# Kernel optimization log

Hardware: AMD Instinct MI355X
Metric: run time of the kernel (lower is better)

Reference implementation:

```python
import jax, jax.numpy as jnp
import numpy as np

DROPOUT_RATE = 0.5
CONF_THRESH = 0.85
IGNORE_VALUE = 2
EPS = 1e-07


def setup_inputs() -> dict:
    key = jax.random.key(0)
    k1, k2 = jax.random.split(key)
    B, H, W = 16, 1024, 1024
    pred = jax.random.uniform(k1, (B, H, W), dtype=jnp.float32)
    mask = jax.random.randint(k2, (B, H, W), 0, 3, dtype=jnp.int32)
    return {"pred": pred, "mask": mask}


def _training_need_score(pred, gt, confidence):
    # Higher = needs more training: CW=4, UW=3, UC=2, CC=1 (+/- confidence bonus)
    is_correct = (pred > 0.5) == (gt == 1.0)
    is_conf = confidence > CONF_THRESH
    score = jnp.where(is_conf & is_correct, 1.0,
            jnp.where(~is_conf & is_correct, 2.0,
            jnp.where(~is_conf & ~is_correct, 3.0, 4.0))).astype(pred.dtype)
    bonus = (confidence - 0.5) * 0.5
    return jnp.where(is_correct, score - bonus, score + bonus)


def _dynamic_masks(pred, mask):
    # Vectorized equivalent of the per-batch nonzero/argsort/scatter loop:
    # rank annotated pixels per batch by descending need-score; top n_train -> train.
    B, H, W = mask.shape
    annotated = (mask != IGNORE_VALUE).reshape(B, H * W)
    gt = mask.astype(pred.dtype)
    confidence = jnp.maximum(pred, 1.0 - pred)
    scores = _training_need_score(pred, gt, confidence).reshape(B, H * W)
    neg_inf = jnp.asarray(-jnp.inf, scores.dtype)
    masked_scores = jnp.where(annotated, scores, neg_inf)
    order = jnp.argsort(-masked_scores, axis=1)          # descending score order
    rank = jnp.argsort(order, axis=1)                    # rank of each pixel in that order
    n_points = annotated.sum(axis=1)
    n_train = (n_points.astype(jnp.float32) * (1.0 - DROPOUT_RATE)).astype(jnp.int32)
    train = annotated & (rank < n_train[:, None])
    holdout = annotated & ~train
    return train.reshape(B, H, W), holdout.reshape(B, H, W)


def reference(pred, mask):
    if pred.ndim == 4 and pred.shape[1] == 1:
        pred = pred[:, 0]
    train_mask, holdout_mask = _dynamic_masks(pred, mask)
    gt = mask.astype(pred.dtype)
    p = jnp.clip(pred, EPS, 1.0 - EPS)
    bce = -(gt * jnp.log(p) + (1.0 - gt) * jnp.log(1.0 - p))
    tm = train_mask.astype(pred.dtype)
    loss = (bce * tm).sum() / (tm.sum() + EPS)
    return loss, train_mask, holdout_mask
```

## Files before the change

kernel.cpp:

```cpp
#include <hip/hip_runtime.h>
#include <stdint.h>

#define NBATCH 16
#define HW_ (1 << 20)
#define TPB 256

#define NBPB_H 32
#define TPB_H 512
#define EPB_H (HW_ / NBPB_H)
#define ITER_H (EPB_H / (TPB_H * 4))

#define NBINS 8192
#define FBASE 0x3F400

#define NBPB_F 256
#define FCHUNK (HW_ / NBPB_F)

#define CAND_CAP 32768
#define LCAP 512
#define TIE_CAP 4096
#define CNT_STRIDE 64

typedef float f4v __attribute__((ext_vector_type(4)));

struct BParams {
    unsigned int k;
    unsigned int bin1f;
    unsigned int r;
    unsigned int mode;
};

__device__ __forceinline__ unsigned int score_bits(float p, int m) {
    bool correct = (p > 0.5f) == (m == 1);
    float conf = fmaxf(p, 1.0f - p);
    float base = correct ? ((conf > 0.85f) ? 1.0f : 2.0f)
                         : ((conf > 0.85f) ? 4.0f : 3.0f);
    float bonus = (conf - 0.5f) * 0.5f;
    float s = correct ? (base - bonus) : (base + bonus);
    return __float_as_uint(s);
}

__global__ void k_hist1(const float4* __restrict__ pred4, const int4* __restrict__ mask4,
                        unsigned int* __restrict__ hist1) {
    __shared__ unsigned int lh[NBINS];
    int b = blockIdx.x / NBPB_H;
    int blk = blockIdx.x % NBPB_H;
    for (int i = threadIdx.x; i < NBINS; i += TPB_H) lh[i] = 0;
    __syncthreads();
    int l4base = blk * (EPB_H / 4);
    for (int j = 0; j < ITER_H; j++) {
        int i4l = l4base + j * TPB_H + threadIdx.x;
        size_t g4 = (size_t)b * (HW_ / 4) + i4l;
        float4 p = pred4[g4];
        int4 m = mask4[g4];
        float pa[4] = {p.x, p.y, p.z, p.w};
        int ma[4] = {m.x, m.y, m.z, m.w};
#pragma unroll
        for (int l = 0; l < 4; l++) {
            if (ma[l] != 2) {
                unsigned int sb = score_bits(pa[l], ma[l]);
                int fb = (int)(sb >> 12) - FBASE;
                fb = min(max(fb, 0), NBINS - 1);
                atomicAdd(&lh[fb], 1u);
            }
        }
    }
    __syncthreads();
    for (int i = threadIdx.x; i < NBINS; i += TPB_H)
        if (lh[i]) atomicAdd(&hist1[b * NBINS + i], lh[i]);
}

__global__ void k_find1(const unsigned int* __restrict__ hist1, BParams* prm) {
    int b = blockIdx.x;
    int t = threadIdx.x;
    __shared__ unsigned int cs_[257];
    const unsigned int* h = hist1 + (size_t)b * NBINS;
    {
        const uint4* h4 = (const uint4*)(h + t * 32);
        unsigned int s = 0;
#pragma unroll
        for (int j = 0; j < 8; j++) { uint4 v = h4[j]; s += v.x + v.y + v.z + v.w; }
        cs_[t] = s;
        if (t == 0) cs_[256] = 0;
    }
    __syncthreads();
    for (int off = 1; off < 256; off <<= 1) {
        unsigned int a = (t + off < 256) ? cs_[t + off] : 0u;
        __syncthreads();
        cs_[t] += a;
        __syncthreads();
    }
    unsigned int n = cs_[0];
    unsigned int k = (unsigned int)(int)((float)n * 0.5f);
    if (k == 0) {
        if (t == 0) {
            BParams P;
            P.k = 0; P.bin1f = 0xFFFFFFFFu; P.r = 0; P.mode = 0;
            prm[b] = P;
        }
        return;
    }
    if (cs_[t] >= k && cs_[t + 1] < k) {
        unsigned int cum = cs_[t + 1];
        for (int j = 31; j >= 0; j--) {
            unsigned int hb = h[t * 32 + j];
            if (cum + hb >= k) {
                BParams P;
                P.k = k;
                P.bin1f = (unsigned int)(FBASE + t * 32 + j);
                P.r = k - cum;
                P.mode = 1;
                prm[b] = P;
                break;
            }
            cum += hb;
        }
    }
}

__global__ void k_main(const float4* __restrict__ pred4, const int4* __restrict__ mask4,
                       const BParams* __restrict__ prm, float* __restrict__ out,
                       float* __restrict__ partials, unsigned int* __restrict__ cand_cnt,
                       unsigned int* __restrict__ cand_idx, unsigned int* __restrict__ cand_sb,
                       float* __restrict__ cand_bce) {
    int b = blockIdx.x / NBPB_F;
    int blk = blockIdx.x % NBPB_F;
    BParams P = prm[b];
    unsigned int target = P.bin1f;
    __shared__ unsigned int lcode[FCHUNK / 4];
    __shared__ float red[TPB];
    __shared__ unsigned int l_idx[LCAP];
    __shared__ unsigned int l_sb[LCAP];
    __shared__ float l_bce[LCAP];
    __shared__ unsigned int lcnt;
    __shared__ unsigned int gbase;
    if (threadIdx.x == 0) lcnt = 0;
    __syncthreads();
    float acc = 0.0f;
    int ibase = blk * FCHUNK;
    for (int j = 0; j < FCHUNK / (TPB * 4); j++) {
        int v = j * TPB + threadIdx.x;
        size_t g4 = (size_t)b * (HW_ / 4) + (ibase / 4) + v;
        float4 p = pred4[g4];
        int4 m = mask4[g4];
        float pa[4] = {p.x, p.y, p.z, p.w};
        int ma[4] = {m.x, m.y, m.z, m.w};
        unsigned int cw = 0;
#pragma unroll
        for (int l = 0; l < 4; l++) {
            bool ann = (ma[l] != 2);
            unsigned int sb = score_bits(pa[l], ma[l]);
            unsigned int fine = sb >> 12;
            bool tr = ann && (fine > target);
            bool amb = ann && (fine == target);
            unsigned int code = (tr ? 1u : 0u) | ((ann && !tr) ? 2u : 0u);
            cw |= code << (8 * l);
            float bce = 0.0f;
            if (tr || amb) {
                float pc = fminf(fmaxf(pa[l], 1e-7f), 1.0f - 1e-7f);
                bce = (ma[l] == 1) ? -__logf(pc) : -__logf(1.0f - pc);
            }
            if (tr) acc += bce;
            if (amb) {
                unsigned int p0 = atomicAdd(&lcnt, 1u);
                if (p0 < LCAP) {
                    l_idx[p0] = (unsigned int)(ibase + v * 4 + l);
                    l_sb[p0] = sb;
                    l_bce[p0] = bce;
                } else {
                    unsigned int gp = atomicAdd(&cand_cnt[b * CNT_STRIDE], 1u);
                    if (gp < CAND_CAP) {
                        size_t o = (size_t)b * CAND_CAP + gp;
                        cand_idx[o] = (unsigned int)(ibase + v * 4 + l);
                        cand_sb[o] = sb;
                        cand_bce[o] = bce;
                    }
                }
            }
        }
        lcode[v] = cw;
    }
    __syncthreads();
    unsigned int n = min(lcnt, (unsigned int)LCAP);
    if (threadIdx.x == 0 && n > 0)
        gbase = atomicAdd(&cand_cnt[b * CNT_STRIDE], n);
    __syncthreads();
    for (unsigned int i = threadIdx.x; i < n; i += TPB) {
        unsigned int pos = gbase + i;
        if (pos < CAND_CAP) {
            size_t o = (size_t)b * CAND_CAP + pos;
            cand_idx[o] = l_idx[i];
            cand_sb[o] = l_sb[i];
            cand_bce[o] = l_bce[i];
        }
    }
    float* trout = out + 1;
    float* hoout = out + 1 + (size_t)NBATCH * HW_;
    size_t Gbase = (size_t)b * HW_ + (size_t)ibase;
    for (int v = threadIdx.x; v < FCHUNK / 4 - 1; v += TPB) {
        unsigned int w0 = lcode[v];
        unsigned int w1 = lcode[v + 1];
        unsigned int c0 = (w0 >> 24) & 0xFFu;
        unsigned int c1 = w1 & 0xFFu;
        unsigned int c2 = (w1 >> 8) & 0xFFu;
        unsigned int c3 = (w1 >> 16) & 0xFFu;
        int e = 3 + 4 * v;
        f4v tv = { (float)(c0 & 1u), (float)(c1 & 1u), (float)(c2 & 1u), (float)(c3 & 1u) };
        f4v hv = { (float)((c0 >> 1) & 1u), (float)((c1 >> 1) & 1u),
                   (float)((c2 >> 1) & 1u), (float)((c3 >> 1) & 1u) };
        __builtin_nontemporal_store(tv, (f4v*)(trout + Gbase + e));
        __builtin_nontemporal_store(hv, (f4v*)(hoout + Gbase + e));
    }
    if (threadIdx.x < 3) {
        unsigned int c = (lcode[0] >> (8 * threadIdx.x)) & 0xFFu;
        trout[Gbase + threadIdx.x] = (float)(c & 1u);
        hoout[Gbase + threadIdx.x] = (float)((c >> 1) & 1u);
    }
    if (threadIdx.x == 3) {
        unsigned int c = (lcode[FCHUNK / 4 - 1] >> 24) & 0xFFu;
        trout[Gbase + FCHUNK - 1] = (float)(c & 1u);
        hoout[Gbase + FCHUNK - 1] = (float)((c >> 1) & 1u);
    }
    red[threadIdx.x] = acc;
    __syncthreads();
    for (int off = TPB / 2; off > 0; off >>= 1) {
        if (threadIdx.x < off) red[threadIdx.x] += red[threadIdx.x + off];
        __syncthreads();
    }
    if (threadIdx.x == 0) partials[blockIdx.x] = red[0];
}

__global__ void k_fixup(const unsigned int* __restrict__ cand_cnt,
                        const unsigned int* __restrict__ cand_idx,
                        const unsigned int* __restrict__ cand_sb,
                        const float* __restrict__ cand_bce,
                        const BParams* __restrict__ prm, float* __restrict__ out,
                        float* __restrict__ tie_partials) {
    int b = blockIdx.x;
    int t = threadIdx.x;
    __shared__ unsigned int h[4096];
    __shared__ unsigned int cs_[257];
    __shared__ unsigned int tie_idx[TIE_CAP];
    __shared__ unsigned int misc[8];
    __shared__ float red[TPB];
    BParams P = prm[b];
    if (P.mode == 0) {
        if (t == 0) tie_partials[b] = 0.0f;
        return;
    }
    unsigned int C = cand_cnt[b * CNT_STRIDE];
    if (C > CAND_CAP) C = CAND_CAP;
    const unsigned int* ci = cand_idx + (size_t)b * CAND_CAP;
    const unsigned int* cs = cand_sb + (size_t)b * CAND_CAP;
    const float* cb = cand_bce + (size_t)b * CAND_CAP;
    for (int i = t; i < 4096; i += TPB) h[i] = 0;
    if (t < 8) misc[t] = (t == 4) ? 0xFFFFFFFFu : 0u;
    __syncthreads();
    for (unsigned int i = t; i < C; i += TPB)
        atomicAdd(&h[cs[i] & 0xFFFu], 1u);
    __syncthreads();
    {
        unsigned int gs = 0;
#pragma unroll
        for (int j = 0; j < 16; j++) gs += h[t * 16 + j];
        cs_[t] = gs;
        if (t == 0) cs_[256] = 0;
    }
    __syncthreads();
    for (int off = 1; off < 256; off <<= 1) {
        unsigned int a = (t + off < 256) ? cs_[t + off] : 0u;
        __syncthreads();
        cs_[t] += a;
        __syncthreads();
    }
    if (cs_[t] >= P.r && cs_[t + 1] < P.r) {
        unsigned int cum = cs_[t + 1];
        for (int j = 15; j >= 0; j--) {
            unsigned int hb = h[t * 16 + j];
            if (cum + hb >= P.r) {
                unsigned int T = P.r - cum;
                misc[0] = (unsigned int)(t * 16 + j);
                misc[1] = T;
                misc[2] = (T == hb) ? 1u : 0u;
                break;
            }
            cum += hb;
        }
    }
    __syncthreads();
    unsigned int vstar = misc[0], T = misc[1];
    bool allTies = (misc[2] != 0);
    unsigned int idxcut;
    if (allTies) {
        idxcut = 0xFFFFFFFFu;
    } else {
        for (unsigned int i = t; i < C; i += TPB) {
            if ((cs[i] & 0xFFFu) == vstar) {
                unsigned int p = atomicAdd(&misc[3], 1u);
                if (p < TIE_CAP) tie_idx[p] = ci[i];
            }
        }
        __syncthreads();
        unsigned int E2 = misc[3];
        if (E2 > TIE_CAP) E2 = TIE_CAP;
        for (unsigned int i = t; i < E2; i += TPB) {
            unsigned int vi = tie_idx[i];
            unsigned int cnt = 0;
            for (unsigned int j = 0; j < E2; j++) cnt += (tie_idx[j] < vi) ? 1u : 0u;
            if (cnt == T - 1) misc[4] = vi;
        }
        __syncthreads();
        idxcut = misc[4];
    }
    float acc = 0.0f;
    float* trout = out + 1;
    float* hoout = out + 1 + (size_t)NBATCH * HW_;
    size_t base = (size_t)b * HW_;
    for (unsigned int i = t; i < C; i += TPB) {
        unsigned int low = cs[i] & 0xFFFu;
        bool tr = (low > vstar) || (low == vstar && ci[i] <= idxcut);
        if (tr) {
            trout[base + ci[i]] = 1.0f;
            hoout[base + ci[i]] = 0.0f;
            acc += cb[i];
        }
    }
    red[t] = acc;
    __syncthreads();
    for (int off = TPB / 2; off > 0; off >>= 1) {
        if (t < off) red[t] += red[t + off];
        __syncthreads();
    }
    if (t == 0) tie_partials[b] = red[0];
}

__global__ void k_loss(const float* __restrict__ partials, const float* __restrict__ tie_partials,
                       const BParams* __restrict__ prm, float* __restrict__ out) {
    __shared__ double red[TPB];
    double s = 0.0;
    for (int i = threadIdx.x; i < NBATCH * NBPB_F; i += TPB) s += (double)partials[i];
    if (threadIdx.x < NBATCH) s += (double)tie_partials[threadIdx.x];
    red[threadIdx.x] = s;
    __syncthreads();
    for (int off = TPB / 2; off > 0; off >>= 1) {
        if (threadIdx.x < off) red[threadIdx.x] += red[threadIdx.x + off];
        __syncthreads();
    }
    if (threadIdx.x == 0) {
        unsigned long long den = 0;
        for (int b = 0; b < NBATCH; b++) den += prm[b].k;
        float denf = (float)den + 1e-7f;
        out[0] = (float)red[0] / denf;
    }
}

extern "C" void kernel_launch(void* const* d_in, const int* in_sizes, int n_in,
                              void* d_out, int out_size, void* d_ws, size_t ws_size,
                              hipStream_t stream) {
    const float4* pred4 = (const float4*)d_in[0];
    const int4* mask4 = (const int4*)d_in[1];
    float* out = (float*)d_out;

    unsigned int* hist1 = (unsigned int*)d_ws;
    unsigned int* cand_cnt = hist1 + NBATCH * NBINS;
    BParams* prm = (BParams*)(cand_cnt + NBATCH * CNT_STRIDE);
    float* partials = (float*)(prm + NBATCH);
    float* tie_partials = partials + NBATCH * NBPB_F;
    unsigned int* cand_idx = (unsigned int*)(tie_partials + NBATCH);
    unsigned int* cand_sb = cand_idx + NBATCH * CAND_CAP;
    float* cand_bce = (float*)(cand_sb + NBATCH * CAND_CAP);

    size_t zero_bytes = (size_t)(NBATCH * NBINS + NBATCH * CNT_STRIDE) * 4;
    hipMemsetAsync(d_ws, 0, zero_bytes, stream);

    k_hist1<<<dim3(NBATCH * NBPB_H), dim3(TPB_H), 0, stream>>>(pred4, mask4, hist1);
    k_find1<<<dim3(NBATCH), dim3(TPB), 0, stream>>>(hist1, prm);
    k_main<<<dim3(NBATCH * NBPB_F), dim3(TPB), 0, stream>>>(pred4, mask4, prm, out, partials,
                                                            cand_cnt, cand_idx, cand_sb, cand_bce);
    k_fixup<<<dim3(NBATCH), dim3(TPB), 0, stream>>>(cand_cnt, cand_idx, cand_sb, cand_bce,
                                                    prm, out, tie_partials);
    k_loss<<<dim3(1), dim3(TPB), 0, stream>>>(partials, tie_partials, prm, out);
}
```

Measured before the change: 286.0 us.

## Fuse find and loss kernels into predecessors via last-block atomic counters

Replaces the separate k_find1 and k_loss launches with last-block-done patterns. The final histogram block of each batch does the threshold search, and the final fixup block does the global loss reduction, using atomic counters and agent-scope loads. It also doubles the histogram blocks per batch to give the pass more parallelism. This removes two kernel launches and their gaps, at the cost of fences, counter atomics and more global histogram atomics.

New measurement: 427.1 us. 49.3% more time.

```diff
diff --git a/kernel.cpp b/kernel.cpp
--- a/kernel.cpp
+++ b/kernel.cpp
@@ -5,7 +5,7 @@
 #define HW_ (1 << 20)
 #define TPB 256
 
-#define NBPB_H 32
+#define NBPB_H 64
 #define TPB_H 512
 #define EPB_H (HW_ / NBPB_H)
 #define ITER_H (EPB_H / (TPB_H * 4))
@@ -40,16 +40,27 @@
     return __float_as_uint(s);
 }
 
+__device__ __forceinline__ unsigned int agent_load_u32(const unsigned int* p) {
+    return __hip_atomic_load(p, __ATOMIC_RELAXED, __HIP_MEMORY_SCOPE_AGENT);
+}
+__device__ __forceinline__ float agent_load_f32(const float* p) {
+    return __hip_atomic_load(p, __ATOMIC_RELAXED, __HIP_MEMORY_SCOPE_AGENT);
+}
+
 __global__ void k_hist1(const float4* __restrict__ pred4, const int4* __restrict__ mask4,
-                        unsigned int* __restrict__ hist1) {
+                        unsigned int* __restrict__ hist1, unsigned int* __restrict__ done_h,
+                        BParams* __restrict__ prm) {
     __shared__ unsigned int lh[NBINS];
+    __shared__ unsigned int cs_[TPB_H + 1];
+    __shared__ unsigned int lasth;
     int b = blockIdx.x / NBPB_H;
     int blk = blockIdx.x % NBPB_H;
-    for (int i = threadIdx.x; i < NBINS; i += TPB_H) lh[i] = 0;
+    int t = threadIdx.x;
+    for (int i = t; i < NBINS; i += TPB_H) lh[i] = 0;
     __syncthreads();
     int l4base = blk * (EPB_H / 4);
     for (int j = 0; j < ITER_H; j++) {
-        int i4l = l4base + j * TPB_H + threadIdx.x;
+        int i4l = l4base + j * TPB_H + t;
         size_t g4 = (size_t)b * (HW_ / 4) + i4l;
         float4 p = pred4[g4];
         int4 m = mask4[g4];
@@ -66,26 +77,25 @@
         }
     }
     __syncthreads();
-    for (int i = threadIdx.x; i < NBINS; i += TPB_H)
+    for (int i = t; i < NBINS; i += TPB_H)
         if (lh[i]) atomicAdd(&hist1[b * NBINS + i], lh[i]);
-}
-
-__global__ void k_find1(const unsigned int* __restrict__ hist1, BParams* prm) {
-    int b = blockIdx.x;
-    int t = threadIdx.x;
-    __shared__ unsigned int cs_[257];
+    __threadfence();
+    __syncthreads();
+    if (t == 0) lasth = (atomicAdd(&done_h[b], 1u) == NBPB_H - 1) ? 1u : 0u;
+    __syncthreads();
+    if (!lasth) return;
+    __threadfence();
     const unsigned int* h = hist1 + (size_t)b * NBINS;
     {
-        const uint4* h4 = (const uint4*)(h + t * 32);
         unsigned int s = 0;
 #pragma unroll
-        for (int j = 0; j < 8; j++) { uint4 v = h4[j]; s += v.x + v.y + v.z + v.w; }
+        for (int j = 0; j < 16; j++) s += agent_load_u32(&h[t * 16 + j]);
         cs_[t] = s;
-        if (t == 0) cs_[256] = 0;
-    }
-    __syncthreads();
-    for (int off = 1; off < 256; off <<= 1) {
-        unsigned int a = (t + off < 256) ? cs_[t + off] : 0u;
+        if (t == 0) cs_[TPB_H] = 0;
+    }
+    __syncthreads();
+    for (int off = 1; off < TPB_H; off <<= 1) {
+        unsigned int a = (t + off < TPB_H) ? cs_[t + off] : 0u;
         __syncthreads();
         cs_[t] += a;
         __syncthreads();
@@ -102,12 +112,12 @@
     }
     if (cs_[t] >= k && cs_[t + 1] < k) {
         unsigned int cum = cs_[t + 1];
-        for (int j = 31; j >= 0; j--) {
-            unsigned int hb = h[t * 32 + j];
+        for (int j = 15; j >= 0; j--) {
+            unsigned int hb = agent_load_u32(&h[t * 16 + j]);
             if (cum + hb >= k) {
                 BParams P;
                 P.k = k;
-                P.bin1f = (unsigned int)(FBASE + t * 32 + j);
+                P.bin1f = (unsigned int)(FBASE + t * 16 + j);
                 P.r = k - cum;
                 P.mode = 1;
                 prm[b] = P;
@@ -235,7 +245,9 @@
                         const unsigned int* __restrict__ cand_sb,
                         const float* __restrict__ cand_bce,
                         const BParams* __restrict__ prm, float* __restrict__ out,
-                        float* __restrict__ tie_partials) {
+                        float* __restrict__ tie_partials,
+                        const float* __restrict__ partials,
+                        unsigned int* __restrict__ done_f) {
     int b = blockIdx.x;
     int t = threadIdx.x;
     __shared__ unsigned int h[4096];
@@ -243,114 +255,118 @@
     __shared__ unsigned int tie_idx[TIE_CAP];
     __shared__ unsigned int misc[8];
     __shared__ float red[TPB];
+    __shared__ double redd[TPB];
+    __shared__ unsigned int lastf;
     BParams P = prm[b];
-    if (P.mode == 0) {
-        if (t == 0) tie_partials[b] = 0.0f;
-        return;
-    }
-    unsigned int C = cand_cnt[b * CNT_STRIDE];
-    if (C > CAND_CAP) C = CAND_CAP;
-    const unsigned int* ci = cand_idx + (size_t)b * CAND_CAP;
-    const unsigned int* cs = cand_sb + (size_t)b * CAND_CAP;
-    const float* cb = cand_bce + (size_t)b * CAND_CAP;
-    for (int i = t; i < 4096; i += TPB) h[i] = 0;
-    if (t < 8) misc[t] = (t == 4) ? 0xFFFFFFFFu : 0u;
-    __syncthreads();
-    for (unsigned int i = t; i < C; i += TPB)
-        atomicAdd(&h[cs[i] & 0xFFFu], 1u);
-    __syncthreads();
-    {
-        unsigned int gs = 0;
+    float tieval = 0.0f;
+    if (P.mode != 0) {
+        unsigned int C = cand_cnt[b * CNT_STRIDE];
+        if (C > CAND_CAP) C = CAND_CAP;
+        const unsigned int* ci = cand_idx + (size_t)b * CAND_CAP;
+        const unsigned int* cs = cand_sb + (size_t)b * CAND_CAP;
+        const float* cb = cand_bce + (size_t)b * CAND_CAP;
+        for (int i = t; i < 4096; i += TPB) h[i] = 0;
+        if (t < 8) misc[t] = (t == 4) ? 0xFFFFFFFFu : 0u;
+        __syncthreads();
+        for (unsigned int i = t; i < C; i += TPB)
+            atomicAdd(&h[cs[i] & 0xFFFu], 1u);
+        __syncthreads();
+        {
+            unsigned int gs = 0;
 #pragma unroll
-        for (int j = 0; j < 16; j++) gs += h[t * 16 + j];
-        cs_[t] = gs;
-        if (t == 0) cs_[256] = 0;
-    }
-    __syncthreads();
-    for (int off = 1; off < 256; off <<= 1) {
-        unsigned int a = (t + off < 256) ? cs_[t + off] : 0u;
-        __syncthreads();
-        cs_[t] += a;
-        __syncthreads();
-    }
-    if (cs_[t] >= P.r && cs_[t + 1] < P.r) {
-        unsigned int cum = cs_[t + 1];
-        for (int j = 15; j >= 0; j--) {
-            unsigned int hb = h[t * 16 + j];
-            if (cum + hb >= P.r) {
-                unsigned int T = P.r - cum;
-                misc[0] = (unsigned int)(t * 16 + j);
-                misc[1] = T;
-                misc[2] = (T == hb) ? 1u : 0u;
-                break;
-            }
-            cum += hb;
-        }
-    }
-    __syncthreads();
-    unsigned int vstar = misc[0], T = misc[1];
-    bool allTies = (misc[2] != 0);
-    unsigned int idxcut;
-    if (allTies) {
-        idxcut = 0xFFFFFFFFu;
-    } else {
+            for (int j = 0; j < 16; j++) gs += h[t * 16 + j];
+            cs_[t] = gs;
+            if (t == 0) cs_[256] = 0;
+        }
+        __syncthreads();
+        for (int off = 1; off < 256; off <<= 1) {
+            unsigned int a = (t + off < 256) ? cs_[t + off] : 0u;
+            __syncthreads();
+            cs_[t] += a;
+            __syncthreads();
+        }
+        if (cs_[t] >= P.r && cs_[t + 1] < P.r) {
+            unsigned int cum = cs_[t + 1];
+            for (int j = 15; j >= 0; j--) {
+                unsigned int hb = h[t * 16 + j];
+                if (cum + hb >= P.r) {
+                    unsigned int T = P.r - cum;
+                    misc[0] = (unsigned int)(t * 16 + j);
+                    misc[1] = T;
+                    misc[2] = (T == hb) ? 1u : 0u;
+                    break;
+                }
+                cum += hb;
+            }
+        }
+        __syncthreads();
+        unsigned int vstar = misc[0], T = misc[1];
+        bool allTies = (misc[2] != 0);
+        unsigned int idxcut;
+        if (allTies) {
+            idxcut = 0xFFFFFFFFu;
+        } else {
+            for (unsigned int i = t; i < C; i += TPB) {
+                if ((cs[i] & 0xFFFu) == vstar) {
+                    unsigned int p = atomicAdd(&misc[3], 1u);
+                    if (p < TIE_CAP) tie_idx[p] = ci[i];
+                }
+            }
+            __syncthreads();
+            unsigned int E2 = misc[3];
+            if (E2 > TIE_CAP) E2 = TIE_CAP;
+            for (unsigned int i = t; i < E2; i += TPB) {
+                unsigned int vi = tie_idx[i];
+                unsigned int cnt = 0;
+                for (unsigned int j = 0; j < E2; j++) cnt += (tie_idx[j] < vi) ? 1u : 0u;
+                if (cnt == T - 1) misc[4] = vi;
+            }
+            __syncthreads();
+            idxcut = misc[4];
+        }
+        float acc = 0.0f;
+        float* trout = out + 1;
+        float* hoout = out + 1 + (size_t)NBATCH * HW_;
+        size_t base = (size_t)b * HW_;
         for (unsigned int i = t; i < C; i += TPB) {
-            if ((cs[i] & 0xFFFu) == vstar) {
-                unsigned int p = atomicAdd(&misc[3], 1u);
-                if (p < TIE_CAP) tie_idx[p] = ci[i];
-            }
-        }
-        __syncthreads();
-        unsigned int E2 = misc[3];
-        if (E2 > TIE_CAP) E2 = TIE_CAP;
-        for (unsigned int i = t; i < E2; i += TPB) {
-            unsigned int vi = tie_idx[i];
-            unsigned int cnt = 0;
-            for (unsigned int j = 0; j < E2; j++) cnt += (tie_idx[j] < vi) ? 1u : 0u;
-            if (cnt == T - 1) misc[4] = vi;
-        }
-        __syncthreads();
-        idxcut = misc[4];
-    }
-    float acc = 0.0f;
-    float* trout = out + 1;
-    float* hoout = out + 1 + (size_t)NBATCH * HW_;
-    size_t base = (size_t)b * HW_;
-    for (unsigned int i = t; i < C; i += TPB) {
-        unsigned int low = cs[i] & 0xFFFu;
-        bool tr = (low > vstar) || (low == vstar && ci[i] <= idxcut);
-        if (tr) {
-            trout[base + ci[i]] = 1.0f;
-            hoout[base + ci[i]] = 0.0f;
-            acc += cb[i];
-        }
-    }
-    red[t] = acc;
+            unsigned int low = cs[i] & 0xFFFu;
+            bool tr = (low > vstar) || (low == vstar && ci[i] <= idxcut);
+            if (tr) {
+                trout[base + ci[i]] = 1.0f;
+                hoout[base + ci[i]] = 0.0f;
+                acc += cb[i];
+            }
+        }
+        red[t] = acc;
+        __syncthreads();
+        for (int off = TPB / 2; off > 0; off >>= 1) {
+            if (t < off) red[t] += red[t + off];
+            __syncthreads();
+        }
+        if (t == 0) tieval = red[0];
+    }
+    if (t == 0)
+        __hip_atomic_store(&tie_partials[b], tieval, __ATOMIC_RELAXED, __HIP_MEMORY_SCOPE_AGENT);
+    __threadfence();
+    __syncthreads();
+    if (t == 0) lastf = (atomicAdd(done_f, 1u) == (unsigned int)(NBATCH - 1)) ? 1u : 0u;
+    __syncthreads();
+    if (!lastf) return;
+    __threadfence();
+    double s = 0.0;
+    for (int i = t; i < NBATCH * NBPB_F; i += TPB) s += (double)partials[i];
+    if (t < NBATCH) s += (double)agent_load_f32(&tie_partials[t]);
+    redd[t] = s;
     __syncthreads();
     for (int off = TPB / 2; off > 0; off >>= 1) {
-        if (t < off) red[t] += red[t + off];
-        __syncthreads();
-    }
-    if (t == 0) tie_partials[b] = red[0];
-}
-
-__global__ void k_loss(const float* __restrict__ partials, const float* __restrict__ tie_partials,
-                       const BParams* __restrict__ prm, float* __restrict__ out) {
-    __shared__ double red[TPB];
-    double s = 0.0;
-    for (int i = threadIdx.x; i < NBATCH * NBPB_F; i += TPB) s += (double)partials[i];
-    if (threadIdx.x < NBATCH) s += (double)tie_partials[threadIdx.x];
-    red[threadIdx.x] = s;
-    __syncthreads();
-    for (int off = TPB / 2; off > 0; off >>= 1) {
-        if (threadIdx.x < off) red[threadIdx.x] += red[threadIdx.x + off];
-        __syncthreads();
-    }
-    if (threadIdx.x == 0) {
+        if (t < off) redd[t] += redd[t + off];
+        __syncthreads();
+    }
+    if (t == 0) {
         unsigned long long den = 0;
-        for (int b = 0; b < NBATCH; b++) den += prm[b].k;
+        for (int b2 = 0; b2 < NBATCH; b2++) den += prm[b2].k;
         float denf = (float)den + 1e-7f;
-        out[0] = (float)red[0] / denf;
+        out[0] = (float)redd[0] / denf;
     }
 }
 
@@ -363,21 +379,21 @@
 
     unsigned int* hist1 = (unsigned int*)d_ws;
     unsigned int* cand_cnt = hist1 + NBATCH * NBINS;
-    BParams* prm = (BParams*)(cand_cnt + NBATCH * CNT_STRIDE);
+    unsigned int* done_h = cand_cnt + NBATCH * CNT_STRIDE;
+    unsigned int* done_f = done_h + NBATCH;
+    BParams* prm = (BParams*)(done_h + 32);
     float* partials = (float*)(prm + NBATCH);
     float* tie_partials = partials + NBATCH * NBPB_F;
     unsigned int* cand_idx = (unsigned int*)(tie_partials + NBATCH);
     unsigned int* cand_sb = cand_idx + NBATCH * CAND_CAP;
     float* cand_bce = (float*)(cand_sb + NBATCH * CAND_CAP);
 
-    size_t zero_bytes = (size_t)(NBATCH * NBINS + NBATCH * CNT_STRIDE) * 4;
+    size_t zero_bytes = (size_t)(NBATCH * NBINS + NBATCH * CNT_STRIDE + 32) * 4;
     hipMemsetAsync(d_ws, 0, zero_bytes, stream);
 
-    k_hist1<<<dim3(NBATCH * NBPB_H), dim3(TPB_H), 0, stream>>>(pred4, mask4, hist1);
-    k_find1<<<dim3(NBATCH), dim3(TPB), 0, stream>>>(hist1, prm);
+    k_hist1<<<dim3(NBATCH * NBPB_H), dim3(TPB_H), 0, stream>>>(pred4, mask4, hist1, done_h, prm);
     k_main<<<dim3(NBATCH * NBPB_F), dim3(TPB), 0, stream>>>(pred4, mask4, prm, out, partials,
                                                             cand_cnt, cand_idx, cand_sb, cand_bce);
     k_fixup<<<dim3(NBATCH), dim3(TPB), 0, stream>>>(cand_cnt, cand_idx, cand_sb, cand_bce,
-                                                    prm, out, tie_partials);
-    k_loss<<<dim3(1), dim3(TPB), 0, stream>>>(partials, tie_partials, prm, out);
-}
+                                                    prm, out, tie_partials, partials, done_f);
+}
```

## Write per-block partial histograms and reduce them in find kernel

Applied to the files above, without the earlier changes.

The histogram kernel now writes each block's shared-memory histogram to its own slice of workspace instead of global atomics into a shared per-batch histogram, and the find kernel sums the 32 partials with 1024 threads before its prefix scan. This removes global atomic contention and most of the memset. The histogram loop is also software-pipelined with register prefetch, and its block size is doubled. The cost is extra global traffic (16×32×8192 words written and read back) done by only 16 blocks in k_find1.

Result: slower. 297.9 us (+4.1%).

```diff
diff --git a/kernel.cpp b/kernel.cpp
--- a/kernel.cpp
+++ b/kernel.cpp
@@ -6,12 +6,14 @@
 #define TPB 256
 
 #define NBPB_H 32
-#define TPB_H 512
+#define TPB_H 1024
 #define EPB_H (HW_ / NBPB_H)
 #define ITER_H (EPB_H / (TPB_H * 4))
 
 #define NBINS 8192
 #define FBASE 0x3F400
+
+#define TPB_F1 1024
 
 #define NBPB_F 256
 #define FCHUNK (HW_ / NBPB_F)
@@ -41,20 +43,26 @@
 }
 
 __global__ void k_hist1(const float4* __restrict__ pred4, const int4* __restrict__ mask4,
-                        unsigned int* __restrict__ hist1) {
+                        unsigned int* __restrict__ hist_part) {
     __shared__ unsigned int lh[NBINS];
     int b = blockIdx.x / NBPB_H;
     int blk = blockIdx.x % NBPB_H;
-    for (int i = threadIdx.x; i < NBINS; i += TPB_H) lh[i] = 0;
-    __syncthreads();
-    int l4base = blk * (EPB_H / 4);
+    int t = threadIdx.x;
+    for (int i = t; i < NBINS; i += TPB_H) lh[i] = 0;
+    __syncthreads();
+    size_t gb = (size_t)b * (HW_ / 4) + (size_t)blk * (EPB_H / 4);
+    float4 p = pred4[gb + t];
+    int4 m = mask4[gb + t];
+#pragma unroll
     for (int j = 0; j < ITER_H; j++) {
-        int i4l = l4base + j * TPB_H + threadIdx.x;
-        size_t g4 = (size_t)b * (HW_ / 4) + i4l;
-        float4 p = pred4[g4];
-        int4 m = mask4[g4];
-        float pa[4] = {p.x, p.y, p.z, p.w};
-        int ma[4] = {m.x, m.y, m.z, m.w};
+        float4 pc = p;
+        int4 mc = m;
+        if (j + 1 < ITER_H) {
+            p = pred4[gb + (size_t)(j + 1) * TPB_H + t];
+            m = mask4[gb + (size_t)(j + 1) * TPB_H + t];
+        }
+        float pa[4] = {pc.x, pc.y, pc.z, pc.w};
+        int ma[4] = {mc.x, mc.y, mc.z, mc.w};
 #pragma unroll
         for (int l = 0; l < 4; l++) {
             if (ma[l] != 2) {
@@ -66,26 +74,31 @@
         }
     }
     __syncthreads();
-    for (int i = threadIdx.x; i < NBINS; i += TPB_H)
-        if (lh[i]) atomicAdd(&hist1[b * NBINS + i], lh[i]);
-}
-
-__global__ void k_find1(const unsigned int* __restrict__ hist1, BParams* prm) {
+    uint4* hp = (uint4*)(hist_part + (size_t)(b * NBPB_H + blk) * NBINS);
+    const uint4* ls = (const uint4*)lh;
+    for (int i4 = t; i4 < NBINS / 4; i4 += TPB_H) hp[i4] = ls[i4];
+}
+
+__global__ void k_find1(const unsigned int* __restrict__ hist_part, BParams* __restrict__ prm) {
     int b = blockIdx.x;
     int t = threadIdx.x;
-    __shared__ unsigned int cs_[257];
-    const unsigned int* h = hist1 + (size_t)b * NBINS;
-    {
-        const uint4* h4 = (const uint4*)(h + t * 32);
-        unsigned int s = 0;
-#pragma unroll
-        for (int j = 0; j < 8; j++) { uint4 v = h4[j]; s += v.x + v.y + v.z + v.w; }
-        cs_[t] = s;
-        if (t == 0) cs_[256] = 0;
-    }
-    __syncthreads();
-    for (int off = 1; off < 256; off <<= 1) {
-        unsigned int a = (t + off < 256) ? cs_[t + off] : 0u;
+    __shared__ unsigned int hs[NBINS];
+    __shared__ unsigned int cs_[TPB_F1 + 1];
+    uint4 a0 = {0, 0, 0, 0}, a1 = {0, 0, 0, 0};
+    for (int p = 0; p < NBPB_H; p++) {
+        const uint4* hp = (const uint4*)(hist_part + (size_t)(b * NBPB_H + p) * NBINS + t * 8);
+        uint4 v0 = hp[0], v1 = hp[1];
+        a0.x += v0.x; a0.y += v0.y; a0.z += v0.z; a0.w += v0.w;
+        a1.x += v1.x; a1.y += v1.y; a1.z += v1.z; a1.w += v1.w;
+    }
+    ((uint4*)hs)[t * 2] = a0;
+    ((uint4*)hs)[t * 2 + 1] = a1;
+    unsigned int s = a0.x + a0.y + a0.z + a0.w + a1.x + a1.y + a1.z + a1.w;
+    cs_[t] = s;
+    if (t == 0) cs_[TPB_F1] = 0;
+    __syncthreads();
+    for (int off = 1; off < TPB_F1; off <<= 1) {
+        unsigned int a = (t + off < TPB_F1) ? cs_[t + off] : 0u;
         __syncthreads();
         cs_[t] += a;
         __syncthreads();
@@ -102,12 +115,12 @@
     }
     if (cs_[t] >= k && cs_[t + 1] < k) {
         unsigned int cum = cs_[t + 1];
-        for (int j = 31; j >= 0; j--) {
-            unsigned int hb = h[t * 32 + j];
+        for (int j = 7; j >= 0; j--) {
+            unsigned int hb = hs[t * 8 + j];
             if (cum + hb >= k) {
                 BParams P;
                 P.k = k;
-                P.bin1f = (unsigned int)(FBASE + t * 32 + j);
+                P.bin1f = (unsigned int)(FBASE + t * 8 + j);
                 P.r = k - cum;
                 P.mode = 1;
                 prm[b] = P;
@@ -361,20 +374,20 @@
     const int4* mask4 = (const int4*)d_in[1];
     float* out = (float*)d_out;
 
-    unsigned int* hist1 = (unsigned int*)d_ws;
-    unsigned int* cand_cnt = hist1 + NBATCH * NBINS;
+    unsigned int* cand_cnt = (unsigned int*)d_ws;
     BParams* prm = (BParams*)(cand_cnt + NBATCH * CNT_STRIDE);
     float* partials = (float*)(prm + NBATCH);
     float* tie_partials = partials + NBATCH * NBPB_F;
     unsigned int* cand_idx = (unsigned int*)(tie_partials + NBATCH);
     unsigned int* cand_sb = cand_idx + NBATCH * CAND_CAP;
     float* cand_bce = (float*)(cand_sb + NBATCH * CAND_CAP);
-
-    size_t zero_bytes = (size_t)(NBATCH * NBINS + NBATCH * CNT_STRIDE) * 4;
+    unsigned int* hist_part = (unsigned int*)(cand_bce + NBATCH * CAND_CAP);
+
+    size_t zero_bytes = (size_t)(NBATCH * CNT_STRIDE) * 4;
     hipMemsetAsync(d_ws, 0, zero_bytes, stream);
 
-    k_hist1<<<dim3(NBATCH * NBPB_H), dim3(TPB_H), 0, stream>>>(pred4, mask4, hist1);
-    k_find1<<<dim3(NBATCH), dim3(TPB), 0, stream>>>(hist1, prm);
+    k_hist1<<<dim3(NBATCH * NBPB_H), dim3(TPB_H), 0, stream>>>(pred4, mask4, hist_part);
+    k_find1<<<dim3(NBATCH), dim3(TPB_F1), 0, stream>>>(hist_part, prm);
     k_main<<<dim3(NBATCH * NBPB_F), dim3(TPB), 0, stream>>>(pred4, mask4, prm, out, partials,
                                                             cand_cnt, cand_idx, cand_sb, cand_bce);
     k_fixup<<<dim3(NBATCH), dim3(TPB), 0, stream>>>(cand_cnt, cand_idx, cand_sb, cand_bce,
```

## Replace global histogram atomics with packed partials, reduce kernel, and prefetch loads

Applied to the files above, without the earlier changes.

The histogram kernel now writes per-block partial histograms packed as 16-bit pairs instead of issuing global atomics, and a new reduce kernel sums them into the final histogram. This removes the large memset of the histogram. Histogram blocks grow to 1024 threads, and both streaming loops software-prefetch the next float4/int4 pair. The mask output stores switch from nontemporal to regular stores. The 16-bit packing assumes each block bin count stays below 65536, which holds because each block handles 32768 elements. The change adds an extra kernel launch and partial-buffer traffic.

New measurement: 289.4 us. About the same (+1.2%).

```diff
diff --git a/kernel.cpp b/kernel.cpp
--- a/kernel.cpp
+++ b/kernel.cpp
@@ -6,12 +6,15 @@
 #define TPB 256
 
 #define NBPB_H 32
-#define TPB_H 512
+#define TPB_H 1024
 #define EPB_H (HW_ / NBPB_H)
 #define ITER_H (EPB_H / (TPB_H * 4))
 
 #define NBINS 8192
 #define FBASE 0x3F400
+
+#define NRED_PB 8
+#define WPB ((NBINS / 2) / NRED_PB)
 
 #define NBPB_F 256
 #define FCHUNK (HW_ / NBPB_F)
@@ -41,20 +44,26 @@
 }
 
 __global__ void k_hist1(const float4* __restrict__ pred4, const int4* __restrict__ mask4,
-                        unsigned int* __restrict__ hist1) {
+                        unsigned int* __restrict__ hist_part16) {
     __shared__ unsigned int lh[NBINS];
     int b = blockIdx.x / NBPB_H;
     int blk = blockIdx.x % NBPB_H;
-    for (int i = threadIdx.x; i < NBINS; i += TPB_H) lh[i] = 0;
-    __syncthreads();
-    int l4base = blk * (EPB_H / 4);
+    int t = threadIdx.x;
+    for (int i = t; i < NBINS; i += TPB_H) lh[i] = 0;
+    __syncthreads();
+    size_t gb = (size_t)b * (HW_ / 4) + (size_t)blk * (EPB_H / 4);
+    float4 p = pred4[gb + t];
+    int4 m = mask4[gb + t];
+#pragma unroll
     for (int j = 0; j < ITER_H; j++) {
-        int i4l = l4base + j * TPB_H + threadIdx.x;
-        size_t g4 = (size_t)b * (HW_ / 4) + i4l;
-        float4 p = pred4[g4];
-        int4 m = mask4[g4];
-        float pa[4] = {p.x, p.y, p.z, p.w};
-        int ma[4] = {m.x, m.y, m.z, m.w};
+        float4 pc = p;
+        int4 mc = m;
+        if (j + 1 < ITER_H) {
+            p = pred4[gb + (size_t)(j + 1) * TPB_H + t];
+            m = mask4[gb + (size_t)(j + 1) * TPB_H + t];
+        }
+        float pa[4] = {pc.x, pc.y, pc.z, pc.w};
+        int ma[4] = {mc.x, mc.y, mc.z, mc.w};
 #pragma unroll
         for (int l = 0; l < 4; l++) {
             if (ma[l] != 2) {
@@ -66,8 +75,30 @@
         }
     }
     __syncthreads();
-    for (int i = threadIdx.x; i < NBINS; i += TPB_H)
-        if (lh[i]) atomicAdd(&hist1[b * NBINS + i], lh[i]);
+    unsigned int* hp = hist_part16 + (size_t)(b * NBPB_H + blk) * (NBINS / 2);
+    for (int w = t; w < NBINS / 2; w += TPB_H)
+        hp[w] = (lh[2 * w] & 0xFFFFu) | (lh[2 * w + 1] << 16);
+}
+
+__global__ void k_reduce(const unsigned int* __restrict__ hist_part16,
+                         unsigned int* __restrict__ hist1) {
+    int b = blockIdx.x / NRED_PB;
+    int sb = blockIdx.x % NRED_PB;
+    int t = threadIdx.x;
+    unsigned int c00 = 0, c01 = 0, c10 = 0, c11 = 0;
+#pragma unroll
+    for (int p = 0; p < NBPB_H; p++) {
+        const unsigned int* hp =
+            hist_part16 + (size_t)(b * NBPB_H + p) * (NBINS / 2) + sb * WPB;
+        unsigned int w0 = hp[t];
+        unsigned int w1 = hp[t + TPB];
+        c00 += w0 & 0xFFFFu; c01 += w0 >> 16;
+        c10 += w1 & 0xFFFFu; c11 += w1 >> 16;
+    }
+    uint2* ob = (uint2*)(hist1 + (size_t)b * NBINS + 2 * (size_t)(sb * WPB));
+    uint2 o0 = {c00, c01}, o1 = {c10, c11};
+    ob[t] = o0;
+    ob[t + TPB] = o1;
 }
 
 __global__ void k_find1(const unsigned int* __restrict__ hist1, BParams* prm) {
@@ -138,13 +169,20 @@
     __syncthreads();
     float acc = 0.0f;
     int ibase = blk * FCHUNK;
+    size_t base4 = (size_t)b * (HW_ / 4) + (size_t)(ibase / 4);
+    float4 p = pred4[base4 + threadIdx.x];
+    int4 m = mask4[base4 + threadIdx.x];
+#pragma unroll
     for (int j = 0; j < FCHUNK / (TPB * 4); j++) {
         int v = j * TPB + threadIdx.x;
-        size_t g4 = (size_t)b * (HW_ / 4) + (ibase / 4) + v;
-        float4 p = pred4[g4];
-        int4 m = mask4[g4];
-        float pa[4] = {p.x, p.y, p.z, p.w};
-        int ma[4] = {m.x, m.y, m.z, m.w};
+        float4 pc = p;
+        int4 mc = m;
+        if (j + 1 < FCHUNK / (TPB * 4)) {
+            p = pred4[base4 + (size_t)(j + 1) * TPB + threadIdx.x];
+            m = mask4[base4 + (size_t)(j + 1) * TPB + threadIdx.x];
+        }
+        float pa[4] = {pc.x, pc.y, pc.z, pc.w};
+        int ma[4] = {mc.x, mc.y, mc.z, mc.w};
         unsigned int cw = 0;
 #pragma unroll
         for (int l = 0; l < 4; l++) {
@@ -157,8 +195,8 @@
             cw |= code << (8 * l);
             float bce = 0.0f;
             if (tr || amb) {
-                float pc = fminf(fmaxf(pa[l], 1e-7f), 1.0f - 1e-7f);
-                bce = (ma[l] == 1) ? -__logf(pc) : -__logf(1.0f - pc);
+                float pc2 = fminf(fmaxf(pa[l], 1e-7f), 1.0f - 1e-7f);
+                bce = (ma[l] == 1) ? -__logf(pc2) : -__logf(1.0f - pc2);
             }
             if (tr) acc += bce;
             if (amb) {
@@ -208,8 +246,8 @@
         f4v tv = { (float)(c0 & 1u), (float)(c1 & 1u), (float)(c2 & 1u), (float)(c3 & 1u) };
         f4v hv = { (float)((c0 >> 1) & 1u), (float)((c1 >> 1) & 1u),
                    (float)((c2 >> 1) & 1u), (float)((c3 >> 1) & 1u) };
-        __builtin_nontemporal_store(tv, (f4v*)(trout + Gbase + e));
-        __builtin_nontemporal_store(hv, (f4v*)(hoout + Gbase + e));
+        *(f4v*)(trout + Gbase + e) = tv;
+        *(f4v*)(hoout + Gbase + e) = hv;
     }
     if (threadIdx.x < 3) {
         unsigned int c = (lcode[0] >> (8 * threadIdx.x)) & 0xFFu;
@@ -361,19 +399,21 @@
     const int4* mask4 = (const int4*)d_in[1];
     float* out = (float*)d_out;
 
-    unsigned int* hist1 = (unsigned int*)d_ws;
-    unsigned int* cand_cnt = hist1 + NBATCH * NBINS;
+    unsigned int* cand_cnt = (unsigned int*)d_ws;
     BParams* prm = (BParams*)(cand_cnt + NBATCH * CNT_STRIDE);
     float* partials = (float*)(prm + NBATCH);
     float* tie_partials = partials + NBATCH * NBPB_F;
     unsigned int* cand_idx = (unsigned int*)(tie_partials + NBATCH);
     unsigned int* cand_sb = cand_idx + NBATCH * CAND_CAP;
     float* cand_bce = (float*)(cand_sb + NBATCH * CAND_CAP);
-
-    size_t zero_bytes = (size_t)(NBATCH * NBINS + NBATCH * CNT_STRIDE) * 4;
+    unsigned int* hist1 = (unsigned int*)(cand_bce + NBATCH * CAND_CAP);
+    unsigned int* hist_part16 = hist1 + NBATCH * NBINS;
+
+    size_t zero_bytes = (size_t)(NBATCH * CNT_STRIDE) * 4;
     hipMemsetAsync(d_ws, 0, zero_bytes, stream);
 
-    k_hist1<<<dim3(NBATCH * NBPB_H), dim3(TPB_H), 0, stream>>>(pred4, mask4, hist1);
+    k_hist1<<<dim3(NBATCH * NBPB_H), dim3(TPB_H), 0, stream>>>(pred4, mask4, hist_part16);
+    k_reduce<<<dim3(NBATCH * NRED_PB), dim3(TPB), 0, stream>>>(hist_part16, hist1);
     k_find1<<<dim3(NBATCH), dim3(TPB), 0, stream>>>(hist1, prm);
     k_main<<<dim3(NBATCH * NBPB_F), dim3(TPB), 0, stream>>>(pred4, mask4, prm, out, partials,
                                                             cand_cnt, cand_idx, cand_sb, cand_bce);
```
